# Performance work log

Measured on AMD Instinct MI355X. Metric: run time of the kernel, lower is better.

## Reference

```python
import jax, jax.numpy as jnp
import numpy as np

BN_EPS = 1e-5
DIST_EPS = 1e-8
K = 3  # fixed 3-NN interpolation


def _cond_conv(x, t_embed, w_t, b_t, w_c, b_c, gamma, beta):
    # time conditioning: GELU(t) -> Linear -> add to channels
    te = jax.nn.gelu(t_embed, approximate=False) @ w_t.T + b_t  # (B, Cin)
    x = x + te[:, :, None]
    # kernel-size-1 Conv1d == channel GEMM
    x = jnp.einsum('oc,bcn->bon', w_c, x) + b_c[None, :, None]
    # BatchNorm1d, training mode: biased stats over (batch, length)
    m = jnp.mean(x, axis=(0, 2), keepdims=True)
    v = jnp.var(x, axis=(0, 2), keepdims=True)
    x = gamma[None, :, None] * (x - m) * jax.lax.rsqrt(v + BN_EPS) + beta[None, :, None]
    return jax.nn.gelu(x, approximate=False)


def _forward(xyz1, xyz2, points1, points2, t_embed,
             w_t1, b_t1, w_c1, b_c1, g1, be1,
             w_t2, b_t2, w_c2, b_c2, g2, be2):
    # squared euclidean distances (cdist**2), computed directly
    # d2[b,n,s] = ||xyz1[b,n]||^2 + ||xyz2[b,s]||^2 - 2 <xyz1[b,n], xyz2[b,s]>
    n1 = jnp.sum(xyz1 * xyz1, axis=-1)  # (B,N)
    n2 = jnp.sum(xyz2 * xyz2, axis=-1)  # (B,S)
    d2 = n1[:, :, None] + n2[:, None, :] - 2.0 * jnp.einsum('bnc,bsc->bns', xyz1, xyz2)
    # top-3 smallest distances (instead of wasteful full sort)
    neg, idx = jax.lax.top_k(-d2, K)        # (B,N,3)
    dists = -neg
    dist_recip = 1.0 / (dists + DIST_EPS)
    weight = dist_recip / jnp.sum(dist_recip, axis=2, keepdims=True)  # (B,N,3)
    pts2t = jnp.transpose(points2, (0, 2, 1))  # (B,S,C2)
    gathered = jax.vmap(lambda p, i: p[i])(pts2t, idx)  # (B,N,3,C2)
    interp = jnp.einsum('bnkc,bnk->bcn', gathered, weight)  # (B,C2,N)
    new_points = jnp.concatenate([points1, interp], axis=1)  # (B,C1+C2,N)
    new_points = _cond_conv(new_points, t_embed, w_t1, b_t1, w_c1, b_c1, g1, be1)
    new_points = _cond_conv(new_points, t_embed, w_t2, b_t2, w_c2, b_c2, g2, be2)
    return new_points


def setup_inputs() -> dict:
    key = jax.random.key(0)
    ks = jax.random.split(key, 12)
    B, N, S, C1, C2, T = 8, 8192, 2048, 128, 256, 256
    Cin = C1 + C2
    s = lambda fan: 1.0 / np.sqrt(fan)
    return {
        'xyz1': jax.random.normal(ks[0], (B, N, 3), jnp.float32),
        'xyz2': jax.random.normal(ks[1], (B, S, 3), jnp.float32),
        'points1': jax.random.normal(ks[2], (B, C1, N), jnp.float32),
        'points2': jax.random.normal(ks[3], (B, C2, S), jnp.float32),
        't_embed': jax.random.normal(ks[4], (B, T), jnp.float32),
        'w_t1': jax.random.normal(ks[5], (Cin, T), jnp.float32) * s(T),
        'b_t1': jnp.zeros((Cin,), jnp.float32),
        'w_c1': jax.random.normal(ks[6], (256, Cin), jnp.float32) * s(Cin),
        'b_c1': jnp.zeros((256,), jnp.float32),
        'g1': jnp.ones((256,), jnp.float32),
        'be1': jnp.zeros((256,), jnp.float32),
        'w_t2': jax.random.normal(ks[7], (256, T), jnp.float32) * s(T),
        'b_t2': jnp.zeros((256,), jnp.float32),
        'w_c2': jax.random.normal(ks[8], (256, 256), jnp.float32) * s(256),
        'b_c2': jnp.zeros((256,), jnp.float32),
        'g2': jnp.ones((256,), jnp.float32),
        'be2': jnp.zeros((256,), jnp.float32),
    }


def reference(xyz1, xyz2, points1, points2, t_embed,
              w_t1, b_t1, w_c1, b_c1, g1, be1,
              w_t2, b_t2, w_c2, b_c2, g2, be2):
    return _forward(xyz1, xyz2, points1, points2, t_embed,
                    w_t1, b_t1, w_c1, b_c1, g1, be1,
                    w_t2, b_t2, w_c2, b_c2, g2, be2)
```

## Files before the change

### kernel.cpp

```cpp
#include <hip/hip_runtime.h>
#include <cfloat>
#include <cmath>

#define B_   8
#define N_   8192
#define S_   2048
#define C1_  128
#define C2_  256
#define T_   256
#define CIN_ 384
#define CO_  256

#define KCH  8
#define KCS  (S_ / KCH)
#define KQB  512

typedef __attribute__((ext_vector_type(8))) short short8;
typedef __attribute__((ext_vector_type(4))) float f32x4;

__device__ __forceinline__ float bf2f(unsigned short u) {
    union { unsigned int i; float f; } v; v.i = ((unsigned int)u) << 16; return v.f;
}
__device__ __forceinline__ unsigned short f2bf(float f) {
    union { float f; unsigned int i; } v; v.f = f;
    unsigned int i = v.i;
    unsigned int r = i + 0x7FFFu + ((i >> 16) & 1u);
    return (unsigned short)(r >> 16);
}
__device__ __forceinline__ float gelu_f(float x) {
    return 0.5f * x * (1.0f + erff(x * 0.70710678118654752440f));
}
__device__ __forceinline__ void async16(const void* g, void* l) {
    __builtin_amdgcn_global_load_lds((const __attribute__((address_space(1))) void*)g,
                                     (__attribute__((address_space(3))) void*)l, 16, 0, 0);
}

#define OFF_TE1   0u
#define OFF_TE2   16384u
#define OFF_BN1   28672u
#define OFF_BN2   30720u
#define OFF_IDX   32768u
#define OFF_WTS   819200u
#define OFF_WC1   1605632u
#define OFF_WC2   1802240u
#define OFF_P2T   2097152u
#define OFF_X1    10485760u
#define OFF_Y     60817408u
#define OFF_PD    OFF_X1
#define OFF_PI    (OFF_X1 + 6291456u)
#define OFF_PS    OFF_P2T
#define OFF_PQ    (OFF_P2T + 1048576u)

__global__ __launch_bounds__(256) void wcvt_kernel(
    const float* __restrict__ w1, const float* __restrict__ w2,
    unsigned short* __restrict__ o1, unsigned short* __restrict__ o2)
{
    int g = blockIdx.x * 256 + threadIdx.x;
    o1[g] = f2bf(w1[g]);
    if (g < CO_ * CO_) o2[g] = f2bf(w2[g]);
}

__global__ __launch_bounds__(640) void te_kernel(
    const float* __restrict__ t_embed,
    const float* __restrict__ w_t1, const float* __restrict__ b_t1,
    const float* __restrict__ w_t2, const float* __restrict__ b_t2,
    float* __restrict__ te1, float* __restrict__ te2)
{
    __shared__ float gt[T_];
    int b = blockIdx.x, t = threadIdx.x;
    if (t < T_) gt[t] = gelu_f(t_embed[b * T_ + t]);
    __syncthreads();
    if (t < CIN_) {
        const float* w = w_t1 + t * T_;
        float s = 0.f;
        for (int k = 0; k < T_; ++k) s += gt[k] * w[k];
        te1[b * CIN_ + t] = s + b_t1[t];
    } else {
        int o = t - CIN_;
        const float* w = w_t2 + o * T_;
        float s = 0.f;
        for (int k = 0; k < T_; ++k) s += gt[k] * w[k];
        te2[b * CO_ + o] = s + b_t2[o];
    }
}

__global__ __launch_bounds__(256) void knn_part_kernel(
    const float* __restrict__ xyz1, const float* __restrict__ xyz2,
    float* __restrict__ pd, int* __restrict__ pi)
{
    __shared__ float4 sp[KCS];
    int b = blockIdx.z, ch = blockIdx.y, tid = threadIdx.x;
    int s0 = ch * KCS;
    {
        int gs = s0 + tid;
        float x = xyz2[(b * S_ + gs) * 3 + 0];
        float y = xyz2[(b * S_ + gs) * 3 + 1];
        float z = xyz2[(b * S_ + gs) * 3 + 2];
        sp[tid] = make_float4(x, y, z, x * x + y * y + z * z);
    }
    __syncthreads();

    float nx[2], ny[2], nz[2], nn[2];
    float d1[2], d2[2], d3[2];
    int   i1[2], i2[2], i3[2];
    #pragma unroll
    for (int qq = 0; qq < 2; ++qq) {
        int n = blockIdx.x * KQB + qq * 256 + tid;
        float x1 = xyz1[(b * N_ + n) * 3 + 0];
        float y1 = xyz1[(b * N_ + n) * 3 + 1];
        float z1 = xyz1[(b * N_ + n) * 3 + 2];
        nn[qq] = x1 * x1 + y1 * y1 + z1 * z1;
        nx[qq] = -2.0f * x1; ny[qq] = -2.0f * y1; nz[qq] = -2.0f * z1;
        d1[qq] = FLT_MAX; d2[qq] = FLT_MAX; d3[qq] = FLT_MAX;
        i1[qq] = 0; i2[qq] = 0; i3[qq] = 0;
    }

    for (int s = 0; s < KCS; s += 4) {
        #pragma unroll
        for (int u = 0; u < 4; ++u) {
            float4 p = sp[s + u];
            int gi = s0 + s + u;
            #pragma unroll
            for (int qq = 0; qq < 2; ++qq) {
                float d = fmaf(nx[qq], p.x,
                          fmaf(ny[qq], p.y,
                          fmaf(nz[qq], p.z, nn[qq] + p.w)));
                bool c3 = d < d3[qq];
                i3[qq] = c3 ? gi : i3[qq];
                d3[qq] = fminf(d3[qq], d);
                bool c2 = d3[qq] < d2[qq];
                float lo2 = fminf(d2[qq], d3[qq]);
                float hi2 = fmaxf(d2[qq], d3[qq]);
                int t2 = c2 ? i3[qq] : i2[qq];
                int t3 = c2 ? i2[qq] : i3[qq];
                d2[qq] = lo2; d3[qq] = hi2; i2[qq] = t2; i3[qq] = t3;
                bool c1 = d2[qq] < d1[qq];
                float lo1 = fminf(d1[qq], d2[qq]);
                float hi1 = fmaxf(d1[qq], d2[qq]);
                int t1  = c1 ? i2[qq] : i1[qq];
                int t2b = c1 ? i1[qq] : i2[qq];
                d1[qq] = lo1; d2[qq] = hi1; i1[qq] = t1; i2[qq] = t2b;
            }
        }
    }

    #pragma unroll
    for (int qq = 0; qq < 2; ++qq) {
        int n = blockIdx.x * KQB + qq * 256 + tid;
        size_t pb = (((size_t)b * KCH + ch) * N_ + n) * 3;
        pd[pb + 0] = d1[qq]; pd[pb + 1] = d2[qq]; pd[pb + 2] = d3[qq];
        pi[pb + 0] = i1[qq]; pi[pb + 1] = i2[qq]; pi[pb + 2] = i3[qq];
    }
}

__global__ __launch_bounds__(256) void knn_merge_kernel(
    const float* __restrict__ pd, const int* __restrict__ pi,
    int* __restrict__ idx, float* __restrict__ wts)
{
    int g = blockIdx.x * 256 + threadIdx.x;
    int b = g >> 13, n = g & (N_ - 1);
    float d1 = FLT_MAX, d2 = FLT_MAX, d3 = FLT_MAX;
    int   i1 = 0, i2 = 0, i3 = 0;
    for (int ch = 0; ch < KCH; ++ch) {
        size_t pb = (((size_t)b * KCH + ch) * N_ + n) * 3;
        #pragma unroll
        for (int k = 0; k < 3; ++k) {
            float d = pd[pb + k];
            int   s = pi[pb + k];
            if (d < d3) {
                if (d < d2) {
                    d3 = d2; i3 = i2;
                    if (d < d1) { d2 = d1; i2 = i1; d1 = d; i1 = s; }
                    else        { d2 = d;  i2 = s; }
                } else { d3 = d; i3 = s; }
            }
        }
    }
    float r1 = 1.0f / (d1 + 1e-8f);
    float r2 = 1.0f / (d2 + 1e-8f);
    float r3 = 1.0f / (d3 + 1e-8f);
    float rs = 1.0f / (r1 + r2 + r3);
    size_t base = (size_t)g * 3;
    idx[base] = i1; idx[base + 1] = i2; idx[base + 2] = i3;
    wts[base] = r1 * rs; wts[base + 1] = r2 * rs; wts[base + 2] = r3 * rs;
}

__global__ __launch_bounds__(256) void transpose_p2(
    const float* __restrict__ p2, unsigned short* __restrict__ p2t)
{
    __shared__ unsigned short tile[32][33];
    int b = blockIdx.z, s0 = blockIdx.x * 32, c0 = blockIdx.y * 32;
    #pragma unroll
    for (int j = 0; j < 4; ++j) {
        int c = threadIdx.y + j * 8;
        tile[c][threadIdx.x] = f2bf(p2[((size_t)b * C2_ + c0 + c) * S_ + s0 + threadIdx.x]);
    }
    __syncthreads();
    #pragma unroll
    for (int j = 0; j < 4; ++j) {
        int s = threadIdx.y + j * 8;
        p2t[((size_t)b * S_ + s0 + s) * C2_ + c0 + threadIdx.x] = tile[threadIdx.x][s];
    }
}

__global__ __launch_bounds__(256) void transpose_p1(
    const float* __restrict__ p1, const float* __restrict__ te1,
    unsigned short* __restrict__ X1)
{
    __shared__ unsigned short tile[32][33];
    int b = blockIdx.z, n0 = blockIdx.x * 32, c0 = blockIdx.y * 32;
    const float* te = te1 + b * CIN_;
    #pragma unroll
    for (int j = 0; j < 4; ++j) {
        int c = threadIdx.y + j * 8;
        tile[c][threadIdx.x] =
            f2bf(p1[((size_t)b * C1_ + c0 + c) * N_ + n0 + threadIdx.x] + te[c0 + c]);
    }
    __syncthreads();
    #pragma unroll
    for (int j = 0; j < 4; ++j) {
        int n = threadIdx.y + j * 8;
        X1[((size_t)b * N_ + n0 + n) * CIN_ + c0 + threadIdx.x] = tile[threadIdx.x][n];
    }
}

__global__ __launch_bounds__(256) void interp_kernel(
    const unsigned short* __restrict__ p2t,
    const int* __restrict__ idx, const float* __restrict__ wts,
    const float* __restrict__ te1, unsigned short* __restrict__ X1)
{
    __shared__ float ste[C2_];
    int tid = threadIdx.x;
    int b = blockIdx.x >> 10;
    ste[tid] = te1[b * CIN_ + C1_ + tid];
    __syncthreads();
    int half = tid >> 5;
    int chunk = tid & 31;
    int gr = blockIdx.x * 8 + half;
    size_t base3 = (size_t)gr * 3;
    int j0 = idx[base3], j1 = idx[base3 + 1], j2 = idx[base3 + 2];
    float w0 = wts[base3], w1 = wts[base3 + 1], w2 = wts[base3 + 2];
    int co = chunk * 8;
    const unsigned short* r0 = p2t + ((size_t)b * S_ + j0) * C2_ + co;
    const unsigned short* r1 = p2t + ((size_t)b * S_ + j1) * C2_ + co;
    const unsigned short* r2 = p2t + ((size_t)b * S_ + j2) * C2_ + co;
    union { short8 v; unsigned short u[8]; } a0, a1, a2, pk;
    a0.v = *(const short8*)r0;
    a1.v = *(const short8*)r1;
    a2.v = *(const short8*)r2;
    #pragma unroll
    for (int jj = 0; jj < 8; ++jj) {
        float v = w0 * bf2f(a0.u[jj]) + w1 * bf2f(a1.u[jj]) + w2 * bf2f(a2.u[jj])
                + ste[co + jj];
        pk.u[jj] = f2bf(v);
    }
    *(short8*)&X1[(size_t)gr * CIN_ + C1_ + co] = pk.v;
}

template <int K, int MODE>
__global__ __launch_bounds__(256) void gemm_bt(
    const unsigned short* __restrict__ A,
    const unsigned short* __restrict__ X,
    const float* __restrict__ bias,
    unsigned short* __restrict__ out,
    float* __restrict__ psum, float* __restrict__ psq)
{
    __shared__ unsigned short sA[128 * 64];
    __shared__ unsigned short sB[128 * 64];
    const int tid = threadIdx.x;
    const int lane = tid & 63, wave = tid >> 6;
    const int wo = wave >> 1, wm = wave & 1;
    const int quad = lane >> 4, col = lane & 15;
    const int b = blockIdx.z;
    const int o0 = blockIdx.y * 128;
    const int n0 = blockIdx.x * 128;
    const unsigned short* Xb = X + (size_t)b * N_ * K;
    const int prow = ((b << 6) + blockIdx.x) * 2 + wm;

    f32x4 acc[4][4];
    #pragma unroll
    for (int i = 0; i < 4; ++i)
        #pragma unroll
        for (int j = 0; j < 4; ++j) acc[i][j] = (f32x4){0.f, 0.f, 0.f, 0.f};

    for (int k0 = 0; k0 < K; k0 += 64) {
        #pragma unroll
        for (int i = 0; i < 4; ++i) {
            int chunk = i * 256 + tid;
            int row = chunk >> 3, c8 = chunk & 7;
            async16(&A [(o0 + row) * K + k0 + c8 * 8], &sA[chunk * 8]);
            async16(&Xb[(size_t)(n0 + row) * K + k0 + c8 * 8], &sB[chunk * 8]);
        }
        __syncthreads();
        #pragma unroll
        for (int kk = 0; kk < 64; kk += 32) {
            short8 af[4], bfr[4];
            #pragma unroll
            for (int i = 0; i < 4; ++i)
                af[i] = *(const short8*)&sA[(wo * 64 + i * 16 + col) * 64 + kk + quad * 8];
            #pragma unroll
            for (int j = 0; j < 4; ++j)
                bfr[j] = *(const short8*)&sB[(wm * 64 + j * 16 + col) * 64 + kk + quad * 8];
            #pragma unroll
            for (int i = 0; i < 4; ++i)
                #pragma unroll
                for (int j = 0; j < 4; ++j)
                    acc[i][j] = __builtin_amdgcn_mfma_f32_16x16x32_bf16(af[i], bfr[j], acc[i][j], 0, 0, 0);
        }
        __syncthreads();
    }

    #pragma unroll
    for (int i = 0; i < 4; ++i) {
        int oo = o0 + wo * 64 + i * 16 + quad * 4;
        float bv0 = bias[oo + 0], bv1 = bias[oo + 1];
        float bv2 = bias[oo + 2], bv3 = bias[oo + 3];
        float s0 = 0.f, s1 = 0.f, s2 = 0.f, s3 = 0.f;
        float q0 = 0.f, q1 = 0.f, q2 = 0.f, q3 = 0.f;
        #pragma unroll
        for (int j = 0; j < 4; ++j) {
            int nn = n0 + wm * 64 + j * 16 + col;
            float v0 = acc[i][j][0] + bv0, v1 = acc[i][j][1] + bv1;
            float v2 = acc[i][j][2] + bv2, v3 = acc[i][j][3] + bv3;
            s0 += v0; q0 += v0 * v0; s1 += v1; q1 += v1 * v1;
            s2 += v2; q2 += v2 * v2; s3 += v3; q3 += v3 * v3;
            if (MODE == 0) {
                union { unsigned short u[4]; uint2 p; } pk;
                pk.u[0] = f2bf(v0); pk.u[1] = f2bf(v1);
                pk.u[2] = f2bf(v2); pk.u[3] = f2bf(v3);
                *(uint2*)&out[((size_t)b * N_ + nn) * CO_ + oo] = pk.p;
            } else {
                out[((size_t)b * CO_ + oo + 0) * N_ + nn] = f2bf(v0);
                out[((size_t)b * CO_ + oo + 1) * N_ + nn] = f2bf(v1);
                out[((size_t)b * CO_ + oo + 2) * N_ + nn] = f2bf(v2);
                out[((size_t)b * CO_ + oo + 3) * N_ + nn] = f2bf(v3);
            }
        }
        #pragma unroll
        for (int off = 1; off < 16; off <<= 1) {
            s0 += __shfl_down(s0, off); q0 += __shfl_down(q0, off);
            s1 += __shfl_down(s1, off); q1 += __shfl_down(q1, off);
            s2 += __shfl_down(s2, off); q2 += __shfl_down(q2, off);
            s3 += __shfl_down(s3, off); q3 += __shfl_down(q3, off);
        }
        if (col == 0) {
            float* ps = psum + (size_t)oo * 1024 + prow;
            float* pq = psq  + (size_t)oo * 1024 + prow;
            ps[0] = s0; ps[1024] = s1; ps[2048] = s2; ps[3072] = s3;
            pq[0] = q0; pq[1024] = q1; pq[2048] = q2; pq[3072] = q3;
        }
    }
}

__global__ __launch_bounds__(256) void bn_reduce_kernel(
    const float* __restrict__ psum, const float* __restrict__ psq,
    const float* __restrict__ gamma, const float* __restrict__ beta,
    float* __restrict__ scale, float* __restrict__ shift)
{
    int ch = blockIdx.x * 8 + (threadIdx.x >> 5);
    int l = threadIdx.x & 31;
    float s = 0.f, q = 0.f;
    for (int r = l; r < 1024; r += 32) {
        s += psum[(size_t)ch * 1024 + r];
        q += psq [(size_t)ch * 1024 + r];
    }
    #pragma unroll
    for (int off = 16; off > 0; off >>= 1) {
        s += __shfl_down(s, off, 32);
        q += __shfl_down(q, off, 32);
    }
    if (l == 0) {
        const float inv = 1.0f / 65536.0f;
        float m = s * inv;
        float var = fmaxf(q * inv - m * m, 0.f);
        float sc = gamma[ch] / sqrtf(var + 1e-5f);
        scale[ch] = sc;
        shift[ch] = beta[ch] - m * sc;
    }
}

__global__ __launch_bounds__(256) void apply1_kernel(
    unsigned short* __restrict__ y, const float* __restrict__ scale,
    const float* __restrict__ shift, const float* __restrict__ te2)
{
    __shared__ float ssc[CO_], ssh[CO_], ste[CO_];
    int b = blockIdx.x >> 10;
    int t = threadIdx.x;
    ssc[t] = scale[t]; ssh[t] = shift[t]; ste[t] = te2[b * CO_ + t];
    __syncthreads();
    int g = blockIdx.x * 256 + t;
    int row = g >> 5;
    int og = (g & 31) * 8;
    unsigned short* p = y + (size_t)row * CO_ + og;
    union { short8 v; unsigned short u[8]; } in, op;
    in.v = *(short8*)p;
    #pragma unroll
    for (int jj = 0; jj < 8; ++jj) {
        int o = og + jj;
        op.u[jj] = f2bf(gelu_f(ssc[o] * bf2f(in.u[jj]) + ssh[o]) + ste[o]);
    }
    *(short8*)p = op.v;
}

__global__ __launch_bounds__(256) void final_kernel(
    const unsigned short* __restrict__ z, const float* __restrict__ scale,
    const float* __restrict__ shift, float* __restrict__ out)
{
    int g = blockIdx.x * 256 + threadIdx.x;
    size_t e = (size_t)g * 8;
    int row = (int)(e >> 13);
    int o = row & (CO_ - 1);
    float sc = scale[o], sh = shift[o];
    union { short8 v; unsigned short u[8]; } in;
    in.v = *(const short8*)&z[e];
    float vo[8];
    #pragma unroll
    for (int jj = 0; jj < 8; ++jj)
        vo[jj] = gelu_f(sc * bf2f(in.u[jj]) + sh);
    *(float4*)&out[e]     = make_float4(vo[0], vo[1], vo[2], vo[3]);
    *(float4*)&out[e + 4] = make_float4(vo[4], vo[5], vo[6], vo[7]);
}

extern "C" void kernel_launch(void* const* d_in, const int* in_sizes, int n_in,
                              void* d_out, int out_size, void* d_ws, size_t ws_size,
                              hipStream_t stream)
{
    (void)in_sizes; (void)n_in; (void)out_size; (void)ws_size;
    const float* xyz1    = (const float*)d_in[0];
    const float* xyz2    = (const float*)d_in[1];
    const float* points1 = (const float*)d_in[2];
    const float* points2 = (const float*)d_in[3];
    const float* t_embed = (const float*)d_in[4];
    const float* w_t1    = (const float*)d_in[5];
    const float* b_t1    = (const float*)d_in[6];
    const float* w_c1    = (const float*)d_in[7];
    const float* b_c1    = (const float*)d_in[8];
    const float* g1      = (const float*)d_in[9];
    const float* be1     = (const float*)d_in[10];
    const float* w_t2    = (const float*)d_in[11];
    const float* b_t2    = (const float*)d_in[12];
    const float* w_c2    = (const float*)d_in[13];
    const float* b_c2    = (const float*)d_in[14];
    const float* g2      = (const float*)d_in[15];
    const float* be2     = (const float*)d_in[16];

    char* w = (char*)d_ws;
    float* te1        = (float*)(w + OFF_TE1);
    float* te2        = (float*)(w + OFF_TE2);
    float* scale1     = (float*)(w + OFF_BN1);
    float* shift1     = scale1 + 256;
    float* scale2     = (float*)(w + OFF_BN2);
    float* shift2     = scale2 + 256;
    int*   idx        = (int*)(w + OFF_IDX);
    float* wts        = (float*)(w + OFF_WTS);
    unsigned short* wc1 = (unsigned short*)(w + OFF_WC1);
    unsigned short* wc2 = (unsigned short*)(w + OFF_WC2);
    unsigned short* p2t = (unsigned short*)(w + OFF_P2T);
    float* pd         = (float*)(w + OFF_PD);
    int*   pi         = (int*)(w + OFF_PI);
    float* psum       = (float*)(w + OFF_PS);
    float* psq        = (float*)(w + OFF_PQ);
    unsigned short* X1  = (unsigned short*)(w + OFF_X1);
    unsigned short* Z   = (unsigned short*)(w + OFF_X1);
    unsigned short* Y   = (unsigned short*)(w + OFF_Y);
    float* out = (float*)d_out;

    hipLaunchKernelGGL(wcvt_kernel, dim3(CIN_ * CO_ / 256), dim3(256), 0, stream,
                       w_c1, w_c2, wc1, wc2);
    hipLaunchKernelGGL(te_kernel, dim3(B_), dim3(640), 0, stream,
                       t_embed, w_t1, b_t1, w_t2, b_t2, te1, te2);
    hipLaunchKernelGGL(knn_part_kernel, dim3(N_ / KQB, KCH, B_), dim3(256), 0, stream,
                       xyz1, xyz2, pd, pi);
    hipLaunchKernelGGL(knn_merge_kernel, dim3(B_ * N_ / 256), dim3(256), 0, stream,
                       pd, pi, idx, wts);
    hipLaunchKernelGGL(transpose_p2, dim3(S_ / 32, C2_ / 32, B_), dim3(32, 8), 0, stream,
                       points2, p2t);
    hipLaunchKernelGGL(transpose_p1, dim3(N_ / 32, C1_ / 32, B_), dim3(32, 8), 0, stream,
                       points1, te1, X1);
    hipLaunchKernelGGL(interp_kernel, dim3(B_ * N_ / 8), dim3(256), 0, stream,
                       p2t, idx, wts, te1, X1);
    hipLaunchKernelGGL((gemm_bt<CIN_, 0>), dim3(N_ / 128, CO_ / 128, B_), dim3(256), 0, stream,
                       wc1, X1, b_c1, Y, psum, psq);
    hipLaunchKernelGGL(bn_reduce_kernel, dim3(32), dim3(256), 0, stream,
                       psum, psq, g1, be1, scale1, shift1);
    hipLaunchKernelGGL(apply1_kernel, dim3(8192), dim3(256), 0, stream,
                       Y, scale1, shift1, te2);
    hipLaunchKernelGGL((gemm_bt<CO_, 1>), dim3(N_ / 128, CO_ / 128, B_), dim3(256), 0, stream,
                       wc2, Y, b_c2, Z, psum, psq);
    hipLaunchKernelGGL(bn_reduce_kernel, dim3(32), dim3(256), 0, stream,
                       psum, psq, g2, be2, scale2, shift2);
    hipLaunchKernelGGL(final_kernel, dim3(8192), dim3(256), 0, stream,
                       Z, scale2, shift2, out);
}
```

Measured before the change: 368.0 us.

## Split KNN over more chunks, cheaper top-3 insert, remap GEMM block order

Doubles the number of KNN source chunks (KCH 8→16) so more blocks run in parallel, and resizes the partial-result buffer to match. Rewrites the per-candidate top-3 insertion as independent compares plus fmed3, and adds the query norm once at the end instead of per candidate. Flattens the GEMM grid into a permuted 1D x index so blocks that share an input tile are scheduled close together for cache reuse. Costs are a longer merge pass over twice as many partials and extra partial-buffer traffic.

```diff
diff --git a/kernel.cpp b/kernel.cpp
--- a/kernel.cpp
+++ b/kernel.cpp
@@ -11,7 +11,7 @@
 #define CIN_ 384
 #define CO_  256
 
-#define KCH  8
+#define KCH  16
 #define KCS  (S_ / KCH)
 #define KQB  512
 
@@ -47,7 +47,7 @@
 #define OFF_X1    10485760u
 #define OFF_Y     60817408u
 #define OFF_PD    OFF_X1
-#define OFF_PI    (OFF_X1 + 6291456u)
+#define OFF_PI    (OFF_X1 + 12582912u)
 #define OFF_PS    OFF_P2T
 #define OFF_PQ    (OFF_P2T + 1048576u)
 
@@ -91,7 +91,7 @@
     __shared__ float4 sp[KCS];
     int b = blockIdx.z, ch = blockIdx.y, tid = threadIdx.x;
     int s0 = ch * KCS;
-    {
+    if (tid < KCS) {
         int gs = s0 + tid;
         float x = xyz2[(b * S_ + gs) * 3 + 0];
         float y = xyz2[(b * S_ + gs) * 3 + 1];
@@ -124,22 +124,20 @@
             for (int qq = 0; qq < 2; ++qq) {
                 float d = fmaf(nx[qq], p.x,
                           fmaf(ny[qq], p.y,
-                          fmaf(nz[qq], p.z, nn[qq] + p.w)));
+                          fmaf(nz[qq], p.z, p.w)));
+                bool c1 = d < d1[qq];
+                bool c2 = d < d2[qq];
                 bool c3 = d < d3[qq];
-                i3[qq] = c3 ? gi : i3[qq];
-                d3[qq] = fminf(d3[qq], d);
-                bool c2 = d3[qq] < d2[qq];
-                float lo2 = fminf(d2[qq], d3[qq]);
-                float hi2 = fmaxf(d2[qq], d3[qq]);
-                int t2 = c2 ? i3[qq] : i2[qq];
-                int t3 = c2 ? i2[qq] : i3[qq];
-                d2[qq] = lo2; d3[qq] = hi2; i2[qq] = t2; i3[qq] = t3;
-                bool c1 = d2[qq] < d1[qq];
-                float lo1 = fminf(d1[qq], d2[qq]);
-                float hi1 = fmaxf(d1[qq], d2[qq]);
-                int t1  = c1 ? i2[qq] : i1[qq];
-                int t2b = c1 ? i1[qq] : i2[qq];
-                d1[qq] = lo1; d2[qq] = hi1; i1[qq] = t1; i2[qq] = t2b;
+                float e1 = fminf(d1[qq], d);
+                float e2 = __builtin_amdgcn_fmed3f(d1[qq], d2[qq], d);
+                float e3 = __builtin_amdgcn_fmed3f(d2[qq], d3[qq], d);
+                int u1  = c1 ? i1[qq] : gi;
+                int n1i = c1 ? gi : i1[qq];
+                int n2i = c2 ? u1 : i2[qq];
+                int u2  = c2 ? i2[qq] : gi;
+                int n3i = c3 ? u2 : i3[qq];
+                d1[qq] = e1; d2[qq] = e2; d3[qq] = e3;
+                i1[qq] = n1i; i2[qq] = n2i; i3[qq] = n3i;
             }
         }
     }
@@ -148,7 +146,9 @@
     for (int qq = 0; qq < 2; ++qq) {
         int n = blockIdx.x * KQB + qq * 256 + tid;
         size_t pb = (((size_t)b * KCH + ch) * N_ + n) * 3;
-        pd[pb + 0] = d1[qq]; pd[pb + 1] = d2[qq]; pd[pb + 2] = d3[qq];
+        pd[pb + 0] = d1[qq] + nn[qq];
+        pd[pb + 1] = d2[qq] + nn[qq];
+        pd[pb + 2] = d3[qq] + nn[qq];
         pi[pb + 0] = i1[qq]; pi[pb + 1] = i2[qq]; pi[pb + 2] = i3[qq];
     }
 }
@@ -272,10 +272,13 @@
     const int wo = wave >> 1, wm = wave & 1;
     const int quad = lane >> 4, col = lane & 15;
     const int b = blockIdx.z;
-    const int o0 = blockIdx.y * 128;
-    const int n0 = blockIdx.x * 128;
+    const int x = blockIdx.x;
+    const int perm = (x & 7) * 16 + (x >> 3);
+    const int n_t = perm >> 1, o_t = perm & 1;
+    const int o0 = o_t * 128;
+    const int n0 = n_t * 128;
     const unsigned short* Xb = X + (size_t)b * N_ * K;
-    const int prow = ((b << 6) + blockIdx.x) * 2 + wm;
+    const int prow = ((b << 6) + n_t) * 2 + wm;
 
     f32x4 acc[4][4];
     #pragma unroll
@@ -479,13 +482,13 @@
                        points1, te1, X1);
     hipLaunchKernelGGL(interp_kernel, dim3(B_ * N_ / 8), dim3(256), 0, stream,
                        p2t, idx, wts, te1, X1);
-    hipLaunchKernelGGL((gemm_bt<CIN_, 0>), dim3(N_ / 128, CO_ / 128, B_), dim3(256), 0, stream,
+    hipLaunchKernelGGL((gemm_bt<CIN_, 0>), dim3(128, 1, B_), dim3(256), 0, stream,
                        wc1, X1, b_c1, Y, psum, psq);
     hipLaunchKernelGGL(bn_reduce_kernel, dim3(32), dim3(256), 0, stream,
                        psum, psq, g1, be1, scale1, shift1);
     hipLaunchKernelGGL(apply1_kernel, dim3(8192), dim3(256), 0, stream,
                        Y, scale1, shift1, te2);
-    hipLaunchKernelGGL((gemm_bt<CO_, 1>), dim3(N_ / 128, CO_ / 128, B_), dim3(256), 0, stream,
+    hipLaunchKernelGGL((gemm_bt<CO_, 1>), dim3(128, 1, B_), dim3(256), 0, stream,
                        wc2, Y, b_c2, Z, psum, psq);
     hipLaunchKernelGGL(bn_reduce_kernel, dim3(32), dim3(256), 0, stream,
                        psum, psq, g2, be2, scale2, shift2);
```

Result: no change. 363.3 us (-1.3%).
